# Optimization experiments

Measured on AMD Instinct MI355X. Metric: run time of the kernel, lower is better.

## Reference

```python
import jax, jax.numpy as jnp
import numpy as np

B, S, EMB, HID, E = 4, 2048, 1024, 2048, 8

def setup_inputs() -> dict:
    key = jax.random.key(0)
    ks = jax.random.split(key, 5)
    scale_g = 1.0 / np.sqrt(EMB)
    x = jax.random.normal(ks[0], (B, S, EMB), dtype=jnp.float32)
    Wg = jax.random.uniform(ks[1], (EMB, E), minval=-scale_g, maxval=scale_g, dtype=jnp.float32)
    bg = jax.random.uniform(ks[2], (E,), minval=-scale_g, maxval=scale_g, dtype=jnp.float32)
    We = jax.random.uniform(ks[3], (E, EMB, HID), minval=-scale_g, maxval=scale_g, dtype=jnp.float32)
    be = jax.random.uniform(ks[4], (E, HID), minval=-scale_g, maxval=scale_g, dtype=jnp.float32)
    return {"x": x, "Wg": Wg, "bg": bg, "We": We, "be": be}

def reference(x, Wg, bg, We, be):
    # gating: softmax over experts, then top-2
    gating_logits = jnp.einsum('bse,ek->bsk', x, Wg) + bg          # [B,S,E]
    gating_weights = jax.nn.softmax(gating_logits, axis=-1)
    top2_weights, top2_indices = jax.lax.top_k(gating_weights, 2)   # [B,S,2]
    # dense all-expert linear (faithful to original naive pattern)
    expert_outputs = jnp.einsum('bse,keh->bskh', x, We) + be        # [B,S,E,H]
    # gather top-2 expert outputs
    top2_expert_outputs = jnp.take_along_axis(
        expert_outputs, top2_indices[..., None], axis=2)            # [B,S,2,H]
    return (top2_weights, top2_expert_outputs)
```

## Files before the change

kernel.cpp:

```cpp
#include <hip/hip_runtime.h>
#include <hip/hip_bf16.h>


#define T_TOKENS 8192
#define EMBD 1024
#define HIDD 2048
#define NEXP 8

#define WS_COUNTS 0
#define WS_NTILES 8
#define WS_TDESC 16
#define WS_EIDS 1024
#define WS_SLOTS 17408

#define X_BF_OFF ((size_t)1 << 20)
#define WE_BF_OFF (X_BF_OFF + (size_t)16777216)
#define WS_NEED (WE_BF_OFF + (size_t)33554432)

typedef __attribute__((ext_vector_type(8))) short short8;
typedef __attribute__((ext_vector_type(4))) float f32x4;

__device__ __forceinline__ unsigned pack2_bf16(float a, float b) {
  unsigned ua = __float_as_uint(a);
  unsigned ub = __float_as_uint(b);
  ua = (ua + 0x7FFFu + ((ua >> 16) & 1u)) >> 16;
  ub = (ub + 0x7FFFu + ((ub >> 16) & 1u)) >> 16;
  return ua | (ub << 16);
}

__device__ __forceinline__ unsigned short bf16_1(float a) {
  unsigned ua = __float_as_uint(a);
  return (unsigned short)((ua + 0x7FFFu + ((ua >> 16) & 1u)) >> 16);
}

typedef __attribute__((address_space(3))) unsigned lds_u32;
typedef const __attribute__((address_space(1))) unsigned glb_u32;
__device__ __forceinline__ void g2lds16(const void* g, void* l) {
  __builtin_amdgcn_global_load_lds((glb_u32*)g, (lds_u32*)l, 16, 0, 0);
}

__global__ __launch_bounds__(256) void gate_kernel(
    const float* __restrict__ x, const float* __restrict__ Wg,
    const float* __restrict__ bg, float* __restrict__ out,
    int* __restrict__ ws) {
  int wid = threadIdx.x >> 6;
  int lane = threadIdx.x & 63;
  int t = blockIdx.x * 4 + wid;
  if (t >= T_TOKENS) return;
  const float* xr = x + (size_t)t * EMBD;
  float acc[8];
#pragma unroll
  for (int e = 0; e < 8; ++e) acc[e] = 0.f;
  for (int i = lane; i < EMBD; i += 64) {
    float xv = xr[i];
    float4 w0 = *(const float4*)(Wg + (size_t)i * 8);
    float4 w1 = *(const float4*)(Wg + (size_t)i * 8 + 4);
    acc[0] += xv * w0.x; acc[1] += xv * w0.y;
    acc[2] += xv * w0.z; acc[3] += xv * w0.w;
    acc[4] += xv * w1.x; acc[5] += xv * w1.y;
    acc[6] += xv * w1.z; acc[7] += xv * w1.w;
  }
#pragma unroll
  for (int off = 32; off > 0; off >>= 1) {
#pragma unroll
    for (int e = 0; e < 8; ++e) acc[e] += __shfl_xor(acc[e], off);
  }
  if (lane == 0) {
    float lg[8];
#pragma unroll
    for (int e = 0; e < 8; ++e) lg[e] = acc[e] + bg[e];
    float mx = lg[0];
#pragma unroll
    for (int e = 1; e < 8; ++e) mx = fmaxf(mx, lg[e]);
    float w[8];
    float s = 0.f;
#pragma unroll
    for (int e = 0; e < 8; ++e) { w[e] = expf(lg[e] - mx); s += w[e]; }
    float inv = 1.f / s;
    int i0 = 0;
#pragma unroll
    for (int e = 1; e < 8; ++e) if (lg[e] > lg[i0]) i0 = e;
    int i1 = (i0 == 0) ? 1 : 0;
#pragma unroll
    for (int e = 0; e < 8; ++e) if (e != i0 && lg[e] > lg[i1]) i1 = e;
    out[(size_t)t * 2] = w[i0] * inv;
    out[(size_t)t * 2 + 1] = w[i1] * inv;
    ws[WS_EIDS + t] = i0 | (i1 << 8);
  }
}

__global__ __launch_bounds__(256) void lists_kernel(int* __restrict__ ws) {
  int e = blockIdx.x;
  int tid = threadIdx.x;
  int lane = tid & 63, wid = tid >> 6;
  __shared__ int wsum[4];
  __shared__ int cursor;
  if (tid == 0) cursor = 0;
  __syncthreads();
  int pk = ws[WS_EIDS + (tid >> 1)];
  for (int it = 0; it < 64; ++it) {
    int s = it * 256 + tid;
    int packed = pk;
    if (it < 63) pk = ws[WS_EIDS + ((s + 256) >> 1)];
    int eid = (s & 1) ? (packed >> 8) : (packed & 255);
    bool f = (eid == e);
    unsigned long long bal = __ballot(f);
    int lpre = __popcll(bal & ((1ull << lane) - 1ull));
    if (lane == 0) wsum[wid] = __popcll(bal);
    __syncthreads();
    int base = 0, tot = 0;
#pragma unroll
    for (int j = 0; j < 4; ++j) {
      int c = wsum[j];
      tot += c;
      if (j < wid) base += c;
    }
    int cur = cursor;
    __syncthreads();
    if (tid == 0) cursor = cur + tot;
    if (f) ws[WS_SLOTS + e * 16384 + cur + base + lpre] = s;
  }
  __syncthreads();
  if (tid == 0) ws[WS_COUNTS + e] = cursor;
}

__global__ void sched_kernel(int* __restrict__ ws, int bm) {
  if (threadIdx.x == 0 && blockIdx.x == 0) {
    int nt = 0;
    for (int e = 0; e < NEXP; ++e) {
      int c = ws[WS_COUNTS + e];
      for (int m0 = 0; m0 < c; m0 += bm) {
        ws[WS_TDESC + nt * 2] = e;
        ws[WS_TDESC + nt * 2 + 1] = m0;
        ++nt;
      }
    }
    ws[WS_NTILES] = nt;
  }
}

__global__ __launch_bounds__(256) void conv_x_kernel(
    const float* __restrict__ x, short* __restrict__ xbf) {
  size_t i8 = ((size_t)blockIdx.x * 256 + threadIdx.x) * 8;
  float4 f0 = *(const float4*)(x + i8);
  float4 f1 = *(const float4*)(x + i8 + 4);
  int4 o;
  o.x = (int)pack2_bf16(f0.x, f0.y);
  o.y = (int)pack2_bf16(f0.z, f0.w);
  o.z = (int)pack2_bf16(f1.x, f1.y);
  o.w = (int)pack2_bf16(f1.z, f1.w);
  *(int4*)(xbf + i8) = o;
}

__global__ __launch_bounds__(256) void conv_wt_kernel(
    const float* __restrict__ We, short* __restrict__ wt) {
  __shared__ float tf[64][65];
  int b = blockIdx.x;
  int e = b >> 9;
  int rem = b & 511;
  int k0 = (rem >> 5) * 64;
  int n0 = (rem & 31) * 64;
  int tid = threadIdx.x;
  const float* src = We + (size_t)e * (EMBD * HIDD) + (size_t)k0 * HIDD + n0;
  int kr = tid >> 4;
  int n4 = (tid & 15) * 4;
#pragma unroll
  for (int ii = 0; ii < 4; ++ii) {
    float4 v = *(const float4*)(src + (size_t)(kr + 16 * ii) * HIDD + n4);
    tf[kr + 16 * ii][n4] = v.x;
    tf[kr + 16 * ii][n4 + 1] = v.y;
    tf[kr + 16 * ii][n4 + 2] = v.z;
    tf[kr + 16 * ii][n4 + 3] = v.w;
  }
  __syncthreads();
  int nr = tid >> 2;
  int kc = (tid & 3) * 16;
  short* dst = wt + (size_t)e * (HIDD * EMBD) + (size_t)(n0 + nr) * EMBD + k0 + kc;
  int4 o0, o1;
  o0.x = (int)pack2_bf16(tf[kc + 0][nr], tf[kc + 1][nr]);
  o0.y = (int)pack2_bf16(tf[kc + 2][nr], tf[kc + 3][nr]);
  o0.z = (int)pack2_bf16(tf[kc + 4][nr], tf[kc + 5][nr]);
  o0.w = (int)pack2_bf16(tf[kc + 6][nr], tf[kc + 7][nr]);
  o1.x = (int)pack2_bf16(tf[kc + 8][nr], tf[kc + 9][nr]);
  o1.y = (int)pack2_bf16(tf[kc + 10][nr], tf[kc + 11][nr]);
  o1.z = (int)pack2_bf16(tf[kc + 12][nr], tf[kc + 13][nr]);
  o1.w = (int)pack2_bf16(tf[kc + 14][nr], tf[kc + 15][nr]);
  *(int4*)dst = o0;
  *(int4*)(dst + 8) = o1;
}

#define MAXMT 136
__global__ __launch_bounds__(256) void expert_gemm_bf16(
    const short* __restrict__ xbf, const short* __restrict__ webf,
    const float* __restrict__ be, const int* __restrict__ ws,
    float* __restrict__ out) {
  __shared__ short lds_s[16384];
  __shared__ int sslot[128];

  int nt = ws[WS_NTILES];
  int bid = blockIdx.x;
  int vid = (bid & 7) * 272 + (bid >> 3);
  int m_idx = vid % MAXMT;
  int n_idx = vid / MAXMT;
  if (m_idx >= nt) return;
  int e = ws[WS_TDESC + m_idx * 2];
  int m0 = ws[WS_TDESC + m_idx * 2 + 1];
  int cnt = ws[WS_COUNTS + e];
  int n0 = n_idx * 128;
  int tid = threadIdx.x;

  if (tid < 128) {
    int slot = -1;
    if (m0 + tid < cnt) slot = ws[WS_SLOTS + e * 16384 + m0 + tid];
    sslot[tid] = slot;
  }
  __syncthreads();

  int srow = tid >> 3;
  int effq = (tid & 7) ^ (srow & 7);
  const short* asrc[4];
  const short* bsrc[4];
  size_t webase = (size_t)e * (HIDD * EMBD);
#pragma unroll
  for (int i = 0; i < 4; ++i) {
    int r = srow + i * 32;
    int slot = sslot[r];
    int tok = (slot >= 0) ? (slot >> 1) : 0;
    asrc[i] = xbf + (size_t)tok * EMBD + effq * 8;
    bsrc[i] = webf + webase + (size_t)(n0 + r) * EMBD + effq * 8;
  }
  short* adst = lds_s + tid * 8;
  short* bdst = lds_s + 8192 + tid * 8;

  int lane = tid & 63, wv = tid >> 6;
  int wr = wv >> 1, wc = wv & 1;
  int lrow = lane & 15, lgrp = lane >> 4;

  f32x4 acc[4][4];
#pragma unroll
  for (int mi = 0; mi < 4; ++mi)
#pragma unroll
    for (int ni = 0; ni < 4; ++ni) acc[mi][ni] = (f32x4){0.f, 0.f, 0.f, 0.f};

#pragma unroll 1
  for (int k0 = 0; k0 < EMBD; k0 += 64) {
#pragma unroll
    for (int i = 0; i < 4; ++i) g2lds16(asrc[i] + k0, adst + i * 2048);
#pragma unroll
    for (int i = 0; i < 4; ++i) g2lds16(bsrc[i] + k0, bdst + i * 2048);
    __syncthreads();
#pragma unroll
    for (int kk = 0; kk < 2; ++kk) {
      short8 a[4], b[4];
#pragma unroll
      for (int mi = 0; mi < 4; ++mi) {
        int row = wr * 64 + mi * 16 + lrow;
        int c = (kk * 4 + lgrp) ^ (row & 7);
        a[mi] = *(const short8*)&lds_s[row * 64 + c * 8];
      }
#pragma unroll
      for (int ni = 0; ni < 4; ++ni) {
        int rn = wc * 64 + ni * 16 + lrow;
        int c = (kk * 4 + lgrp) ^ (rn & 7);
        b[ni] = *(const short8*)&lds_s[8192 + rn * 64 + c * 8];
      }
#pragma unroll
      for (int mi = 0; mi < 4; ++mi)
#pragma unroll
        for (int ni = 0; ni < 4; ++ni)
          acc[mi][ni] =
              __builtin_amdgcn_mfma_f32_16x16x32_bf16(a[mi], b[ni], acc[mi][ni], 0, 0, 0);
    }
    __syncthreads();
  }

#pragma unroll
  for (int ni = 0; ni < 4; ++ni) {
    int colg = n0 + wc * 64 + ni * 16 + lrow;
    float bev = be[(size_t)e * HIDD + colg];
#pragma unroll
    for (int mi = 0; mi < 4; ++mi) {
#pragma unroll
      for (int r = 0; r < 4; ++r) {
        int m = wr * 64 + mi * 16 + lgrp * 4 + r;
        int slot = sslot[m];
        if (slot >= 0)
          out[(size_t)T_TOKENS * 2 + (size_t)slot * HIDD + colg] =
              acc[mi][ni][r] + bev;
      }
    }
  }
}

#define BMF 64
#define LDT 72
__global__ __launch_bounds__(256) void expert_kernel_f32(
    const float* __restrict__ x, const float* __restrict__ We,
    const float* __restrict__ be, const int* __restrict__ ws,
    float* __restrict__ out) {
  __shared__ short As[BMF * LDT];
  __shared__ short Bs[64 * LDT];
  __shared__ int sslot[BMF];

  int nt = ws[WS_NTILES];
  if ((int)blockIdx.x >= nt) return;
  int e = ws[WS_TDESC + blockIdx.x * 2];
  int m0 = ws[WS_TDESC + blockIdx.x * 2 + 1];
  int cnt = ws[WS_COUNTS + e];
  int n0 = blockIdx.y * 64;

  int tid = threadIdx.x;
  if (tid < BMF) {
    int slot = -1;
    if (m0 + tid < cnt) slot = ws[WS_SLOTS + e * 16384 + m0 + tid];
    sslot[tid] = slot;
  }
  __syncthreads();

  int lane = tid & 63;
  int wid = tid >> 6;
  int wr = wid >> 1, wc = wid & 1;
  int lrow = lane & 15, lgrp = lane >> 4;

  f32x4 acc[2][2];
#pragma unroll
  for (int mi = 0; mi < 2; ++mi)
#pragma unroll
    for (int ni = 0; ni < 2; ++ni) acc[mi][ni] = (f32x4){0.f, 0.f, 0.f, 0.f};

  int arow = tid >> 2;
  int acq = (tid & 3) * 16;
  int aslot = sslot[arow];
  const float* abase = (aslot >= 0) ? (x + (size_t)(aslot >> 1) * EMBD + acq) : x;
  int bk = tid >> 2;
  int bnq = (tid & 3) * 16;
  const float* wbase = We + (size_t)e * EMBD * HIDD + (size_t)bk * HIDD + n0 + bnq;

#pragma unroll 1
  for (int ks = 0; ks < EMBD / 64; ++ks) {
    int k0 = ks * 64;
    {
      unsigned pk[8];
      if (aslot >= 0) {
        const float4* p = (const float4*)(abase + k0);
        float4 f0 = p[0], f1 = p[1], f2 = p[2], f3 = p[3];
        pk[0] = pack2_bf16(f0.x, f0.y); pk[1] = pack2_bf16(f0.z, f0.w);
        pk[2] = pack2_bf16(f1.x, f1.y); pk[3] = pack2_bf16(f1.z, f1.w);
        pk[4] = pack2_bf16(f2.x, f2.y); pk[5] = pack2_bf16(f2.z, f2.w);
        pk[6] = pack2_bf16(f3.x, f3.y); pk[7] = pack2_bf16(f3.z, f3.w);
      } else {
#pragma unroll
        for (int i = 0; i < 8; ++i) pk[i] = 0u;
      }
      int4* dst = (int4*)&As[arow * LDT + acq];
      dst[0] = make_int4((int)pk[0], (int)pk[1], (int)pk[2], (int)pk[3]);
      dst[1] = make_int4((int)pk[4], (int)pk[5], (int)pk[6], (int)pk[7]);
    }
    {
      const float4* p = (const float4*)(wbase + (size_t)k0 * HIDD);
      float4 f0 = p[0], f1 = p[1], f2 = p[2], f3 = p[3];
      float v[16] = {f0.x, f0.y, f0.z, f0.w, f1.x, f1.y, f1.z, f1.w,
                     f2.x, f2.y, f2.z, f2.w, f3.x, f3.y, f3.z, f3.w};
#pragma unroll
      for (int j = 0; j < 16; ++j) Bs[(bnq + j) * LDT + bk] = (short)bf16_1(v[j]);
    }
    __syncthreads();
#pragma unroll
    for (int kk = 0; kk < 2; ++kk) {
      short8 a0 = *(const short8*)&As[(wr * 32 + 0 + lrow) * LDT + kk * 32 + lgrp * 8];
      short8 a1 = *(const short8*)&As[(wr * 32 + 16 + lrow) * LDT + kk * 32 + lgrp * 8];
      short8 b0 = *(const short8*)&Bs[(wc * 32 + 0 + lrow) * LDT + kk * 32 + lgrp * 8];
      short8 b1 = *(const short8*)&Bs[(wc * 32 + 16 + lrow) * LDT + kk * 32 + lgrp * 8];
      acc[0][0] = __builtin_amdgcn_mfma_f32_16x16x32_bf16(a0, b0, acc[0][0], 0, 0, 0);
      acc[0][1] = __builtin_amdgcn_mfma_f32_16x16x32_bf16(a0, b1, acc[0][1], 0, 0, 0);
      acc[1][0] = __builtin_amdgcn_mfma_f32_16x16x32_bf16(a1, b0, acc[1][0], 0, 0, 0);
      acc[1][1] = __builtin_amdgcn_mfma_f32_16x16x32_bf16(a1, b1, acc[1][1], 0, 0, 0);
    }
    __syncthreads();
  }

#pragma unroll
  for (int ni = 0; ni < 2; ++ni) {
    int colg = n0 + wc * 32 + ni * 16 + lrow;
    float bev = be[(size_t)e * HIDD + colg];
#pragma unroll
    for (int mi = 0; mi < 2; ++mi) {
#pragma unroll
      for (int r = 0; r < 4; ++r) {
        int m = wr * 32 + mi * 16 + lgrp * 4 + r;
        int slot = sslot[m];
        if (slot >= 0)
          out[(size_t)T_TOKENS * 2 + (size_t)slot * HIDD + colg] =
              acc[mi][ni][r] + bev;
      }
    }
  }
}

extern "C" void kernel_launch(void* const* d_in, const int* in_sizes, int n_in,
                              void* d_out, int out_size, void* d_ws,
                              size_t ws_size, hipStream_t stream) {
  const float* x = (const float*)d_in[0];
  const float* Wg = (const float*)d_in[1];
  const float* bg = (const float*)d_in[2];
  const float* We = (const float*)d_in[3];
  const float* be = (const float*)d_in[4];
  float* out = (float*)d_out;
  int* ws = (int*)d_ws;

  bool fast = ws_size >= WS_NEED;

  gate_kernel<<<T_TOKENS / 4, 256, 0, stream>>>(x, Wg, bg, out, ws);
  lists_kernel<<<NEXP, 256, 0, stream>>>(ws);
  sched_kernel<<<1, 64, 0, stream>>>(ws, fast ? 128 : 64);

  if (fast) {
    short* xbf = (short*)((char*)d_ws + X_BF_OFF);
    short* webf = (short*)((char*)d_ws + WE_BF_OFF);
    conv_x_kernel<<<4096, 256, 0, stream>>>(x, xbf);
    conv_wt_kernel<<<4096, 256, 0, stream>>>(We, webf);
    expert_gemm_bf16<<<MAXMT * 16, 256, 0, stream>>>(xbf, webf, be, ws, out);
  } else {
    expert_kernel_f32<<<dim3(264, 32), 256, 0, stream>>>(x, We, be, ws, out);
  }
}
```

Measured before the change: 422.2 us.

## Fuse x conversion into gating, replace list/sched kernels with atomic scatter

Folds the fp32-to-bf16 conversion of x into the gate kernel and replaces the serial lists_kernel and single-thread sched_kernel with a parallel atomic-based scatter kernel. Each GEMM block now derives its expert and row offset from the per-expert counts, and the fp32 fallback path is removed. This cuts kernel launches and the serialized list-building work. In exchange, token order within each expert list becomes nondeterministic, and the workspace is now assumed to be large enough.

Result: faster. 401.8 us (-4.8%).

```diff
diff --git a/kernel.cpp b/kernel.cpp
--- a/kernel.cpp
+++ b/kernel.cpp
@@ -8,14 +8,15 @@
 #define NEXP 8
 
 #define WS_COUNTS 0
-#define WS_NTILES 8
-#define WS_TDESC 16
 #define WS_EIDS 1024
 #define WS_SLOTS 17408
 
 #define X_BF_OFF ((size_t)1 << 20)
 #define WE_BF_OFF (X_BF_OFF + (size_t)16777216)
 #define WS_NEED (WE_BF_OFF + (size_t)33554432)
+
+#define MAXMT 135
+#define NTILE 16
 
 typedef __attribute__((ext_vector_type(8))) short short8;
 typedef __attribute__((ext_vector_type(4))) float f32x4;
@@ -28,11 +29,6 @@
   return ua | (ub << 16);
 }
 
-__device__ __forceinline__ unsigned short bf16_1(float a) {
-  unsigned ua = __float_as_uint(a);
-  return (unsigned short)((ua + 0x7FFFu + ((ua >> 16) & 1u)) >> 16);
-}
-
 typedef __attribute__((address_space(3))) unsigned lds_u32;
 typedef const __attribute__((address_space(1))) unsigned glb_u32;
 __device__ __forceinline__ void g2lds16(const void* g, void* l) {
@@ -42,15 +38,15 @@
 __global__ __launch_bounds__(256) void gate_kernel(
     const float* __restrict__ x, const float* __restrict__ Wg,
     const float* __restrict__ bg, float* __restrict__ out,
-    int* __restrict__ ws) {
+    int* __restrict__ ws, short* __restrict__ xbf) {
   int wid = threadIdx.x >> 6;
   int lane = threadIdx.x & 63;
   int t = blockIdx.x * 4 + wid;
-  if (t >= T_TOKENS) return;
   const float* xr = x + (size_t)t * EMBD;
   float acc[8];
 #pragma unroll
   for (int e = 0; e < 8; ++e) acc[e] = 0.f;
+#pragma unroll 4
   for (int i = lane; i < EMBD; i += 64) {
     float xv = xr[i];
     float4 w0 = *(const float4*)(Wg + (size_t)i * 8);
@@ -87,69 +83,38 @@
     out[(size_t)t * 2 + 1] = w[i1] * inv;
     ws[WS_EIDS + t] = i0 | (i1 << 8);
   }
-}
-
-__global__ __launch_bounds__(256) void lists_kernel(int* __restrict__ ws) {
-  int e = blockIdx.x;
-  int tid = threadIdx.x;
-  int lane = tid & 63, wid = tid >> 6;
-  __shared__ int wsum[4];
-  __shared__ int cursor;
-  if (tid == 0) cursor = 0;
-  __syncthreads();
-  int pk = ws[WS_EIDS + (tid >> 1)];
-  for (int it = 0; it < 64; ++it) {
-    int s = it * 256 + tid;
-    int packed = pk;
-    if (it < 63) pk = ws[WS_EIDS + ((s + 256) >> 1)];
-    int eid = (s & 1) ? (packed >> 8) : (packed & 255);
+  const float* xc = xr + lane * 16;
+  float4 f0 = *(const float4*)(xc);
+  float4 f1 = *(const float4*)(xc + 4);
+  float4 f2 = *(const float4*)(xc + 8);
+  float4 f3 = *(const float4*)(xc + 12);
+  int4 o0, o1;
+  o0.x = (int)pack2_bf16(f0.x, f0.y); o0.y = (int)pack2_bf16(f0.z, f0.w);
+  o0.z = (int)pack2_bf16(f1.x, f1.y); o0.w = (int)pack2_bf16(f1.z, f1.w);
+  o1.x = (int)pack2_bf16(f2.x, f2.y); o1.y = (int)pack2_bf16(f2.z, f2.w);
+  o1.z = (int)pack2_bf16(f3.x, f3.y); o1.w = (int)pack2_bf16(f3.z, f3.w);
+  short* dst = xbf + (size_t)t * EMBD + lane * 16;
+  *(int4*)dst = o0;
+  *(int4*)(dst + 8) = o1;
+}
+
+__global__ __launch_bounds__(256) void scatter_kernel(int* __restrict__ ws) {
+  int s = blockIdx.x * 256 + threadIdx.x;
+  int lane = threadIdx.x & 63;
+  int packed = ws[WS_EIDS + (s >> 1)];
+  int eid = (s & 1) ? ((packed >> 8) & 255) : (packed & 255);
+#pragma unroll
+  for (int e = 0; e < 8; ++e) {
     bool f = (eid == e);
     unsigned long long bal = __ballot(f);
-    int lpre = __popcll(bal & ((1ull << lane) - 1ull));
-    if (lane == 0) wsum[wid] = __popcll(bal);
-    __syncthreads();
-    int base = 0, tot = 0;
-#pragma unroll
-    for (int j = 0; j < 4; ++j) {
-      int c = wsum[j];
-      tot += c;
-      if (j < wid) base += c;
-    }
-    int cur = cursor;
-    __syncthreads();
-    if (tid == 0) cursor = cur + tot;
-    if (f) ws[WS_SLOTS + e * 16384 + cur + base + lpre] = s;
-  }
-  __syncthreads();
-  if (tid == 0) ws[WS_COUNTS + e] = cursor;
-}
-
-__global__ void sched_kernel(int* __restrict__ ws, int bm) {
-  if (threadIdx.x == 0 && blockIdx.x == 0) {
-    int nt = 0;
-    for (int e = 0; e < NEXP; ++e) {
-      int c = ws[WS_COUNTS + e];
-      for (int m0 = 0; m0 < c; m0 += bm) {
-        ws[WS_TDESC + nt * 2] = e;
-        ws[WS_TDESC + nt * 2 + 1] = m0;
-        ++nt;
-      }
-    }
-    ws[WS_NTILES] = nt;
-  }
-}
-
-__global__ __launch_bounds__(256) void conv_x_kernel(
-    const float* __restrict__ x, short* __restrict__ xbf) {
-  size_t i8 = ((size_t)blockIdx.x * 256 + threadIdx.x) * 8;
-  float4 f0 = *(const float4*)(x + i8);
-  float4 f1 = *(const float4*)(x + i8 + 4);
-  int4 o;
-  o.x = (int)pack2_bf16(f0.x, f0.y);
-  o.y = (int)pack2_bf16(f0.z, f0.w);
-  o.z = (int)pack2_bf16(f1.x, f1.y);
-  o.w = (int)pack2_bf16(f1.z, f1.w);
-  *(int4*)(xbf + i8) = o;
+    if (bal) {
+      int lpre = __popcll(bal & ((1ull << lane) - 1ull));
+      int base = 0;
+      if (lane == 0) base = atomicAdd(&ws[WS_COUNTS + e * 16], __popcll(bal));
+      base = __shfl(base, 0);
+      if (f) ws[WS_SLOTS + e * 16384 + base + lpre] = s;
+    }
+  }
 }
 
 __global__ __launch_bounds__(256) void conv_wt_kernel(
@@ -189,7 +154,6 @@
   *(int4*)(dst + 8) = o1;
 }
 
-#define MAXMT 136
 __global__ __launch_bounds__(256) void expert_gemm_bf16(
     const short* __restrict__ xbf, const short* __restrict__ webf,
     const float* __restrict__ be, const int* __restrict__ ws,
@@ -197,15 +161,23 @@
   __shared__ short lds_s[16384];
   __shared__ int sslot[128];
 
-  int nt = ws[WS_NTILES];
   int bid = blockIdx.x;
-  int vid = (bid & 7) * 272 + (bid >> 3);
+  int vid = (bid & 7) * (MAXMT * NTILE / 8) + (bid >> 3);
   int m_idx = vid % MAXMT;
   int n_idx = vid / MAXMT;
-  if (m_idx >= nt) return;
-  int e = ws[WS_TDESC + m_idx * 2];
-  int m0 = ws[WS_TDESC + m_idx * 2 + 1];
-  int cnt = ws[WS_COUNTS + e];
+
+  int e = -1, m0 = 0, cnt = 0;
+  {
+    int acc = 0;
+#pragma unroll
+    for (int ee = 0; ee < 8; ++ee) {
+      int c = ws[WS_COUNTS + ee * 16];
+      int nte = (c + 127) >> 7;
+      if (e < 0 && m_idx < acc + nte) { e = ee; m0 = (m_idx - acc) * 128; cnt = c; }
+      acc += nte;
+    }
+  }
+  if (e < 0) return;
   int n0 = n_idx * 128;
   int tid = threadIdx.x;
 
@@ -268,8 +240,8 @@
       for (int mi = 0; mi < 4; ++mi)
 #pragma unroll
         for (int ni = 0; ni < 4; ++ni)
-          acc[mi][ni] =
-              __builtin_amdgcn_mfma_f32_16x16x32_bf16(a[mi], b[ni], acc[mi][ni], 0, 0, 0);
+          acc[mi][ni] = __builtin_amdgcn_mfma_f32_16x16x32_bf16(
+              a[mi], b[ni], acc[mi][ni], 0, 0, 0);
     }
     __syncthreads();
   }
@@ -283,111 +255,6 @@
 #pragma unroll
       for (int r = 0; r < 4; ++r) {
         int m = wr * 64 + mi * 16 + lgrp * 4 + r;
-        int slot = sslot[m];
-        if (slot >= 0)
-          out[(size_t)T_TOKENS * 2 + (size_t)slot * HIDD + colg] =
-              acc[mi][ni][r] + bev;
-      }
-    }
-  }
-}
-
-#define BMF 64
-#define LDT 72
-__global__ __launch_bounds__(256) void expert_kernel_f32(
-    const float* __restrict__ x, const float* __restrict__ We,
-    const float* __restrict__ be, const int* __restrict__ ws,
-    float* __restrict__ out) {
-  __shared__ short As[BMF * LDT];
-  __shared__ short Bs[64 * LDT];
-  __shared__ int sslot[BMF];
-
-  int nt = ws[WS_NTILES];
-  if ((int)blockIdx.x >= nt) return;
-  int e = ws[WS_TDESC + blockIdx.x * 2];
-  int m0 = ws[WS_TDESC + blockIdx.x * 2 + 1];
-  int cnt = ws[WS_COUNTS + e];
-  int n0 = blockIdx.y * 64;
-
-  int tid = threadIdx.x;
-  if (tid < BMF) {
-    int slot = -1;
-    if (m0 + tid < cnt) slot = ws[WS_SLOTS + e * 16384 + m0 + tid];
-    sslot[tid] = slot;
-  }
-  __syncthreads();
-
-  int lane = tid & 63;
-  int wid = tid >> 6;
-  int wr = wid >> 1, wc = wid & 1;
-  int lrow = lane & 15, lgrp = lane >> 4;
-
-  f32x4 acc[2][2];
-#pragma unroll
-  for (int mi = 0; mi < 2; ++mi)
-#pragma unroll
-    for (int ni = 0; ni < 2; ++ni) acc[mi][ni] = (f32x4){0.f, 0.f, 0.f, 0.f};
-
-  int arow = tid >> 2;
-  int acq = (tid & 3) * 16;
-  int aslot = sslot[arow];
-  const float* abase = (aslot >= 0) ? (x + (size_t)(aslot >> 1) * EMBD + acq) : x;
-  int bk = tid >> 2;
-  int bnq = (tid & 3) * 16;
-  const float* wbase = We + (size_t)e * EMBD * HIDD + (size_t)bk * HIDD + n0 + bnq;
-
-#pragma unroll 1
-  for (int ks = 0; ks < EMBD / 64; ++ks) {
-    int k0 = ks * 64;
-    {
-      unsigned pk[8];
-      if (aslot >= 0) {
-        const float4* p = (const float4*)(abase + k0);
-        float4 f0 = p[0], f1 = p[1], f2 = p[2], f3 = p[3];
-        pk[0] = pack2_bf16(f0.x, f0.y); pk[1] = pack2_bf16(f0.z, f0.w);
-        pk[2] = pack2_bf16(f1.x, f1.y); pk[3] = pack2_bf16(f1.z, f1.w);
-        pk[4] = pack2_bf16(f2.x, f2.y); pk[5] = pack2_bf16(f2.z, f2.w);
-        pk[6] = pack2_bf16(f3.x, f3.y); pk[7] = pack2_bf16(f3.z, f3.w);
-      } else {
-#pragma unroll
-        for (int i = 0; i < 8; ++i) pk[i] = 0u;
-      }
-      int4* dst = (int4*)&As[arow * LDT + acq];
-      dst[0] = make_int4((int)pk[0], (int)pk[1], (int)pk[2], (int)pk[3]);
-      dst[1] = make_int4((int)pk[4], (int)pk[5], (int)pk[6], (int)pk[7]);
-    }
-    {
-      const float4* p = (const float4*)(wbase + (size_t)k0 * HIDD);
-      float4 f0 = p[0], f1 = p[1], f2 = p[2], f3 = p[3];
-      float v[16] = {f0.x, f0.y, f0.z, f0.w, f1.x, f1.y, f1.z, f1.w,
-                     f2.x, f2.y, f2.z, f2.w, f3.x, f3.y, f3.z, f3.w};
-#pragma unroll
-      for (int j = 0; j < 16; ++j) Bs[(bnq + j) * LDT + bk] = (short)bf16_1(v[j]);
-    }
-    __syncthreads();
-#pragma unroll
-    for (int kk = 0; kk < 2; ++kk) {
-      short8 a0 = *(const short8*)&As[(wr * 32 + 0 + lrow) * LDT + kk * 32 + lgrp * 8];
-      short8 a1 = *(const short8*)&As[(wr * 32 + 16 + lrow) * LDT + kk * 32 + lgrp * 8];
-      short8 b0 = *(const short8*)&Bs[(wc * 32 + 0 + lrow) * LDT + kk * 32 + lgrp * 8];
-      short8 b1 = *(const short8*)&Bs[(wc * 32 + 16 + lrow) * LDT + kk * 32 + lgrp * 8];
-      acc[0][0] = __builtin_amdgcn_mfma_f32_16x16x32_bf16(a0, b0, acc[0][0], 0, 0, 0);
-      acc[0][1] = __builtin_amdgcn_mfma_f32_16x16x32_bf16(a0, b1, acc[0][1], 0, 0, 0);
-      acc[1][0] = __builtin_amdgcn_mfma_f32_16x16x32_bf16(a1, b0, acc[1][0], 0, 0, 0);
-      acc[1][1] = __builtin_amdgcn_mfma_f32_16x16x32_bf16(a1, b1, acc[1][1], 0, 0, 0);
-    }
-    __syncthreads();
-  }
-
-#pragma unroll
-  for (int ni = 0; ni < 2; ++ni) {
-    int colg = n0 + wc * 32 + ni * 16 + lrow;
-    float bev = be[(size_t)e * HIDD + colg];
-#pragma unroll
-    for (int mi = 0; mi < 2; ++mi) {
-#pragma unroll
-      for (int r = 0; r < 4; ++r) {
-        int m = wr * 32 + mi * 16 + lgrp * 4 + r;
         int slot = sslot[m];
         if (slot >= 0)
           out[(size_t)T_TOKENS * 2 + (size_t)slot * HIDD + colg] =
@@ -407,20 +274,12 @@
   const float* be = (const float*)d_in[4];
   float* out = (float*)d_out;
   int* ws = (int*)d_ws;
-
-  bool fast = ws_size >= WS_NEED;
-
-  gate_kernel<<<T_TOKENS / 4, 256, 0, stream>>>(x, Wg, bg, out, ws);
-  lists_kernel<<<NEXP, 256, 0, stream>>>(ws);
-  sched_kernel<<<1, 64, 0, stream>>>(ws, fast ? 128 : 64);
-
-  if (fast) {
-    short* xbf = (short*)((char*)d_ws + X_BF_OFF);
-    short* webf = (short*)((char*)d_ws + WE_BF_OFF);
-    conv_x_kernel<<<4096, 256, 0, stream>>>(x, xbf);
-    conv_wt_kernel<<<4096, 256, 0, stream>>>(We, webf);
-    expert_gemm_bf16<<<MAXMT * 16, 256, 0, stream>>>(xbf, webf, be, ws, out);
-  } else {
-    expert_kernel_f32<<<dim3(264, 32), 256, 0, stream>>>(x, We, be, ws, out);
-  }
-}
+  short* xbf = (short*)((char*)d_ws + X_BF_OFF);
+  short* webf = (short*)((char*)d_ws + WE_BF_OFF);
+
+  hipMemsetAsync(d_ws, 0, 1024, stream);
+  gate_kernel<<<T_TOKENS / 4, 256, 0, stream>>>(x, Wg, bg, out, ws, xbf);
+  scatter_kernel<<<64, 256, 0, stream>>>(ws);
+  conv_wt_kernel<<<4096, 256, 0, stream>>>(We, webf);
+  expert_gemm_bf16<<<MAXMT * NTILE, 256, 0, stream>>>(xbf, webf, be, ws, out);
+}
```
